# Optimization experiments

Hardware: AMD Instinct MI355X
Metric: run time of the kernel (lower is better)

## Reference

```python
import jax, jax.numpy as jnp
import numpy as np


def setup_inputs() -> dict:
    key = jax.random.key(0)
    k1, k2 = jax.random.split(key)
    B, C, H, W = 8, 21, 512, 512
    inp = jax.random.normal(k1, (B, C, H, W), dtype=jnp.float32)
    target = jax.random.randint(k2, (B, H, W), 0, C, dtype=jnp.int64)
    return {"input": inp, "target": target}


def reference(input, target):
    # input: (B, C, H, W) logits; target: (B, H, W) int labels in [0, C)
    B, C, H, W = input.shape
    N = H * W
    logits = input.reshape(B, C, N)                      # (B, C, N)
    tgt = target.reshape(B, N)                           # (B, N)
    tgt_f = tgt.astype(logits.dtype)

    probs = jax.nn.softmax(logits, axis=1)               # (B, C, N)
    # foreground mask per class: (B, C, N)
    fg = (tgt[:, None, :] == jnp.arange(C)[None, :, None]).astype(logits.dtype)
    errors = jnp.abs(fg - probs)                         # (B, C, N)

    # descending sort along N, vectorized over all (B, C) rows
    perm = jnp.argsort(-errors, axis=2)                  # (B, C, N)
    errors_sorted = jnp.take_along_axis(errors, perm, axis=2)
    # faithful to kornia: gather the raw float labels (not the binary mask)
    tgt_bc = jnp.broadcast_to(tgt_f[:, None, :], (B, C, N))
    target_sorted = jnp.take_along_axis(tgt_bc, perm, axis=2)  # (B, C, N)

    tsum = jnp.sum(target_sorted, axis=2, keepdims=True)       # (B, C, 1)
    intersection = tsum - jnp.cumsum(target_sorted, axis=2)
    union = tsum + jnp.cumsum(1.0 - target_sorted, axis=2)
    gradient = 1.0 - intersection / union                      # (B, C, N)
    # in-place diff along last axis: g[..., 1:] -= g[..., :-1]
    gradient = jnp.concatenate(
        [gradient[..., :1], gradient[..., 1:] - gradient[..., :-1]], axis=-1
    )

    # per-class loss = mean over batch of sum over pixels; final = mean over classes
    loss_bc = jnp.sum(jax.nn.relu(errors_sorted) * gradient, axis=2)  # (B, C)
    return jnp.mean(loss_bc)
```

## Files before the change

### kernel.cpp

```cpp
#include <hip/hip_runtime.h>


#define NB     8
#define NC     21
#define NPIX   262144
#define NROWS  (NB * NC)
#define NBINS  768
#define CHUNKS 64
#define CHUNK  (NPIX / CHUNKS)

__device__ __forceinline__ void bin_px(float xv, float Lq, unsigned lab, int c,
                                       unsigned* hist) {
  float p = __expf(xv - Lq);
  float e = fabsf((((int)lab == c) ? 1.0f : 0.0f) - p);
  unsigned fb = __float_as_uint(e);
  int      fx = (int)(fb >> 23) - 127;
  unsigned k;
  if (fx < -12) k = 0u;
  else {
    k = (((unsigned)(fx + 12)) << 6) | ((fb >> 17) & 63u);
    if (k > NBINS - 1) k = NBINS - 1;
  }
  atomicAdd(hist + k, (1u << 18) | lab);
}

__global__ __launch_bounds__(1024, 8) void k_fused(
    const float* __restrict__ x,
    const int* __restrict__ tgt,
    unsigned* __restrict__ partial) {
  __shared__ float    Ls[CHUNK];
  __shared__ unsigned hist[NBINS];
  int tid = threadIdx.x;
  for (int i = tid; i < NBINS; i += 1024) hist[i] = 0;

  int b     = blockIdx.x >> 6;
  int chunk = blockIdx.x & 63;
  const float* xb = x + (size_t)b * NC * NPIX + (size_t)chunk * CHUNK;
  const int*   tb = tgt + (size_t)b * NPIX + (size_t)chunk * CHUNK;

  int n4 = tid * 4;

  float Z0 = 0.f, Z1 = 0.f, Z2 = 0.f, Z3 = 0.f;
  #pragma unroll
  for (int c = 0; c < NC; ++c) {
    float4 t = *(const float4*)(xb + (size_t)c * NPIX + n4);
    Z0 += __expf(t.x); Z1 += __expf(t.y); Z2 += __expf(t.z); Z3 += __expf(t.w);
  }
  float4 Lv;
  Lv.x = __logf(Z0); Lv.y = __logf(Z1); Lv.z = __logf(Z2); Lv.w = __logf(Z3);
  *(float4*)(Ls + n4) = Lv;

  int4 tv = *(const int4*)(tb + n4);
  unsigned tl = (unsigned)tv.x | ((unsigned)tv.y << 8) |
                ((unsigned)tv.z << 16) | ((unsigned)tv.w << 24);
  __syncthreads();

  unsigned* op = partial + (size_t)blockIdx.x * NC * NBINS;
  for (int c = 0; c < NC; ++c) {
    float4 t  = *(const float4*)(xb + (size_t)c * NPIX + n4);
    float4 Lq = *(const float4*)(Ls + n4);
    bin_px(t.x, Lq.x,  tl        & 255u, c, hist);
    bin_px(t.y, Lq.y, (tl >>  8) & 255u, c, hist);
    bin_px(t.z, Lq.z, (tl >> 16) & 255u, c, hist);
    bin_px(t.w, Lq.w, (tl >> 24) & 255u, c, hist);
    __syncthreads();
    for (int i = tid; i < NBINS; i += 1024) {
      op[(size_t)c * NBINS + i] = hist[i];
      hist[i] = 0;
    }
    __syncthreads();
  }
}

__device__ inline unsigned long long shfl_up_u64(unsigned long long v, int off) {
  unsigned lo = (unsigned)v, hi = (unsigned)(v >> 32);
  lo = (unsigned)__shfl_up((int)lo, off, 64);
  hi = (unsigned)__shfl_up((int)hi, off, 64);
  return ((unsigned long long)hi << 32) | lo;
}
__device__ inline unsigned long long shfl_down_u64(unsigned long long v, int off) {
  unsigned lo = (unsigned)v, hi = (unsigned)(v >> 32);
  lo = (unsigned)__shfl_down((int)lo, off, 64);
  hi = (unsigned)__shfl_down((int)hi, off, 64);
  return ((unsigned long long)hi << 32) | lo;
}

__global__ __launch_bounds__(768) void k_scan(
    const unsigned* __restrict__ partial,
    float* __restrict__ out) {
  int row  = blockIdx.x;
  int b    = row / NC;
  int c    = row - b * NC;
  int tid  = threadIdx.x;
  int lane = tid & 63;
  int wave = tid >> 6;

  __shared__ unsigned long long hist0[NBINS];
  __shared__ unsigned long long wtot[12];
  __shared__ double wred[12];
  __shared__ double sT;

  {
    const unsigned* pp = partial + ((size_t)(b * CHUNKS) * NC + c) * NBINS + tid;
    unsigned long long cnt = 0, ls = 0;
    #pragma unroll 8
    for (int j = 0; j < CHUNKS; ++j) {
      unsigned v = pp[(size_t)j * NC * NBINS];
      cnt += (v >> 18);
      ls  += (v & 0x3FFFFu);
    }
    hist0[tid] = (cnt << 32) | ls;
  }
  __syncthreads();

  unsigned long long tot = hist0[tid];
  #pragma unroll
  for (int off = 32; off > 0; off >>= 1) tot += shfl_down_u64(tot, off);
  if (lane == 0) wtot[wave] = tot;
  __syncthreads();
  if (tid == 0) {
    unsigned long long g = 0;
    #pragma unroll
    for (int w = 0; w < 12; ++w) g += wtot[w];
    sT = (double)(unsigned)(g & 0xffffffffULL);
  }
  __syncthreads();
  double T = sT;
  __syncthreads();

  int bin = (NBINS - 1) - tid;
  unsigned long long v = hist0[bin];

  unsigned long long s = v;
  #pragma unroll
  for (int off = 1; off < 64; off <<= 1) {
    unsigned long long u = shfl_up_u64(s, off);
    if (lane >= off) s += u;
  }
  if (lane == 63) wtot[wave] = s;
  __syncthreads();

  unsigned long long woff = 0;
  for (int w = 0; w < wave; ++w) woff += wtot[w];
  unsigned long long excl = s - v + woff;

  double acc = 0.0;
  unsigned n = (unsigned)(v >> 32);
  if (n) {
    unsigned sl = (unsigned)(v & 0xffffffffu);
    unsigned cb = (unsigned)(excl >> 32);
    unsigned sb = (unsigned)(excl & 0xffffffffu);
    double Sb = (double)sb + (double)sl;
    double gb = 1.0 - (T - Sb) / (T + (double)(cb + n) - Sb);
    double ga = (cb == 0) ? 0.0
                          : 1.0 - (T - (double)sb) / (T + (double)cb - (double)sb);
    unsigned key = (unsigned)bin;
    unsigned ex  = key >> 6, mant = key & 63u;
    float e = ldexpf(1.0f + ((float)mant + 0.5f) * 0.015625f, (int)ex - 12);
    acc = (double)e * (gb - ga);
  }

  #pragma unroll
  for (int off = 32; off > 0; off >>= 1) acc += __shfl_down(acc, off, 64);
  if (lane == 0) wred[wave] = acc;
  __syncthreads();
  if (tid == 0) {
    double ssum = 0.0;
    #pragma unroll
    for (int w = 0; w < 12; ++w) ssum += wred[w];
    atomicAdd(out, (float)(ssum * (1.0 / (double)NROWS)));
  }
}

extern "C" void kernel_launch(void* const* d_in, const int* in_sizes, int n_in,
                              void* d_out, int out_size, void* d_ws, size_t ws_size,
                              hipStream_t stream) {
  const float* x  = (const float*)d_in[0];
  const int* tgt  = (const int*)d_in[1];
  float* out      = (float*)d_out;
  unsigned* partial = (unsigned*)d_ws;

  hipMemsetAsync(d_out, 0, sizeof(float), stream);
  k_fused<<<NB * CHUNKS, 1024, 0, stream>>>(x, tgt, partial);
  k_scan<<<NROWS, NBINS, 0, stream>>>(partial, out);
}
```

Baseline: 283.8 us.

## Give each class its own shared histogram and split class work across waves

The fused kernel now keeps all 21 per-class histograms in shared memory at once. This removes the two block-wide barriers per class and the per-class flush loop. Waves take (class, half-chunk) work items and software-prefetch their float4 loads, and the log-sum-exp is kept in shared memory as fp16 in base-2 form. Bin computation is simplified to a single shift and clamp. The cost is much larger shared memory (about 63KB), which lowers occupancy. The fp16 logsumexp also loses precision, which could shift bin assignment.

```diff
diff --git a/kernel.cpp b/kernel.cpp
--- a/kernel.cpp
+++ b/kernel.cpp
@@ -8,68 +8,77 @@
 #define NBINS  768
 #define CHUNKS 64
 #define CHUNK  (NPIX / CHUNKS)
-
-__device__ __forceinline__ void bin_px(float xv, float Lq, unsigned lab, int c,
-                                       unsigned* hist) {
-  float p = __expf(xv - Lq);
-  float e = fabsf((((int)lab == c) ? 1.0f : 0.0f) - p);
-  unsigned fb = __float_as_uint(e);
-  int      fx = (int)(fb >> 23) - 127;
-  unsigned k;
-  if (fx < -12) k = 0u;
-  else {
-    k = (((unsigned)(fx + 12)) << 6) | ((fb >> 17) & 63u);
-    if (k > NBINS - 1) k = NBINS - 1;
-  }
-  atomicAdd(hist + k, (1u << 18) | lab);
-}
+#define LOG2E  1.4426950408889634f
 
 __global__ __launch_bounds__(1024, 8) void k_fused(
     const float* __restrict__ x,
     const int* __restrict__ tgt,
     unsigned* __restrict__ partial) {
-  __shared__ float    Ls[CHUNK];
-  __shared__ unsigned hist[NBINS];
-  int tid = threadIdx.x;
-  for (int i = tid; i < NBINS; i += 1024) hist[i] = 0;
+  __shared__ unsigned      hist[NC * NBINS];
+  __shared__ _Float16      Ls[CHUNK];
+  __shared__ unsigned char labs[CHUNK];
 
+  int tid   = threadIdx.x;
   int b     = blockIdx.x >> 6;
   int chunk = blockIdx.x & 63;
   const float* xb = x + (size_t)b * NC * NPIX + (size_t)chunk * CHUNK;
-  const int*   tb = tgt + (size_t)b * NPIX + (size_t)chunk * CHUNK;
+
+  for (int i = tid; i < NC * NBINS; i += 1024) hist[i] = 0;
 
   int n4 = tid * 4;
-
   float Z0 = 0.f, Z1 = 0.f, Z2 = 0.f, Z3 = 0.f;
   #pragma unroll
   for (int c = 0; c < NC; ++c) {
     float4 t = *(const float4*)(xb + (size_t)c * NPIX + n4);
-    Z0 += __expf(t.x); Z1 += __expf(t.y); Z2 += __expf(t.z); Z3 += __expf(t.w);
+    Z0 += exp2f(t.x * LOG2E);
+    Z1 += exp2f(t.y * LOG2E);
+    Z2 += exp2f(t.z * LOG2E);
+    Z3 += exp2f(t.w * LOG2E);
   }
-  float4 Lv;
-  Lv.x = __logf(Z0); Lv.y = __logf(Z1); Lv.z = __logf(Z2); Lv.w = __logf(Z3);
-  *(float4*)(Ls + n4) = Lv;
+  Ls[n4 + 0] = (_Float16)__log2f(Z0);
+  Ls[n4 + 1] = (_Float16)__log2f(Z1);
+  Ls[n4 + 2] = (_Float16)__log2f(Z2);
+  Ls[n4 + 3] = (_Float16)__log2f(Z3);
+  {
+    int4 tv = *(const int4*)(tgt + (size_t)b * NPIX + (size_t)chunk * CHUNK + n4);
+    *(unsigned*)(labs + n4) = (unsigned)tv.x | ((unsigned)tv.y << 8) |
+                              ((unsigned)tv.z << 16) | ((unsigned)tv.w << 24);
+  }
+  __syncthreads();
 
-  int4 tv = *(const int4*)(tb + n4);
-  unsigned tl = (unsigned)tv.x | ((unsigned)tv.y << 8) |
-                ((unsigned)tv.z << 16) | ((unsigned)tv.w << 24);
+  int wave = tid >> 6, lane = tid & 63;
+  struct H4 { _Float16 v[4]; };
+  for (int ii = wave; ii < 2 * NC; ii += 16) {
+    int c = ii >> 1, h = ii & 1;
+    const float* xc = xb + (size_t)c * NPIX + h * 2048;
+    unsigned* hc = hist + c * NBINS;
+
+    float4 nxt = *(const float4*)(xc + lane * 4);
+    #pragma unroll
+    for (int it = 0; it < 8; ++it) {
+      float4 cur = nxt;
+      if (it < 7) nxt = *(const float4*)(xc + (it + 1) * 256 + lane * 4);
+      int px = h * 2048 + it * 256 + lane * 4;
+      H4 l4 = *(const H4*)(Ls + px);
+      unsigned lb = *(const unsigned*)(labs + px);
+      float xs[4] = {cur.x, cur.y, cur.z, cur.w};
+      #pragma unroll
+      for (int j = 0; j < 4; ++j) {
+        float L2q = (float)l4.v[j];
+        float p   = exp2f(fmaf(xs[j], LOG2E, -L2q));
+        unsigned lab = (lb >> (8 * j)) & 255u;
+        float sel = ((int)lab == c) ? 1.0f : 0.0f;
+        float e   = fabsf(sel - p);
+        int k = (int)(__float_as_uint(e) >> 17) - 7360;
+        k = min(max(k, 0), NBINS - 1);
+        atomicAdd(hc + k, (1u << 18) | lab);
+      }
+    }
+  }
   __syncthreads();
 
   unsigned* op = partial + (size_t)blockIdx.x * NC * NBINS;
-  for (int c = 0; c < NC; ++c) {
-    float4 t  = *(const float4*)(xb + (size_t)c * NPIX + n4);
-    float4 Lq = *(const float4*)(Ls + n4);
-    bin_px(t.x, Lq.x,  tl        & 255u, c, hist);
-    bin_px(t.y, Lq.y, (tl >>  8) & 255u, c, hist);
-    bin_px(t.z, Lq.z, (tl >> 16) & 255u, c, hist);
-    bin_px(t.w, Lq.w, (tl >> 24) & 255u, c, hist);
-    __syncthreads();
-    for (int i = tid; i < NBINS; i += 1024) {
-      op[(size_t)c * NBINS + i] = hist[i];
-      hist[i] = 0;
-    }
-    __syncthreads();
-  }
+  for (int i = tid; i < NC * NBINS; i += 1024) op[i] = hist[i];
 }
 
 __device__ inline unsigned long long shfl_up_u64(unsigned long long v, int off) {
```

After: 282.5 us. About the same (-0.5%).
